# Optimization experiments

Measured on AMD Instinct MI355X. Metric: run time of the kernel, lower is better.

The kernel has to match this reference:

```python
import jax, jax.numpy as jnp
import numpy as np

C = 768
H = 12
T = 4096
B = 1
EPS = 1e-5


def setup_inputs() -> dict:
    key = jax.random.key(0)
    ks = jax.random.split(key, 16)
    s = 0.02
    return {
        "x": jax.random.normal(ks[0], (B, T, C), jnp.float32),
        "ln1_w": jnp.ones((C,), jnp.float32),
        "ln1_b": jnp.zeros((C,), jnp.float32),
        "W_attn": jax.random.normal(ks[1], (C, 3 * C), jnp.float32) * s,
        "b_attn": jnp.zeros((3 * C,), jnp.float32),
        "W_proj": jax.random.normal(ks[2], (C, C), jnp.float32) * s,
        "b_proj": jnp.zeros((C,), jnp.float32),
        "ln2_w": jnp.ones((C,), jnp.float32),
        "ln2_b": jnp.zeros((C,), jnp.float32),
        "W_fc": jax.random.normal(ks[3], (C, 4 * C), jnp.float32) * s,
        "b_fc": jnp.zeros((4 * C,), jnp.float32),
        "W_fc2": jax.random.normal(ks[4], (4 * C, C), jnp.float32) * s,
        "b_fc2": jnp.zeros((C,), jnp.float32),
    }


def _layernorm(x, w, b):
    mu = jnp.mean(x, axis=-1, keepdims=True)
    var = jnp.var(x, axis=-1, keepdims=True)
    return (x - mu) * jax.lax.rsqrt(var + EPS) * w + b


def _attn(x, W_attn, b_attn, W_proj, b_proj):
    Bb, Tt, Cc = x.shape
    hd = Cc // H
    qkv = x @ W_attn + b_attn                       # (B,T,3C)
    q, k, v = jnp.split(qkv, 3, axis=-1)
    q = q.reshape(Bb, Tt, H, hd).transpose(0, 2, 1, 3)  # (B,H,T,hd)
    k = k.reshape(Bb, Tt, H, hd).transpose(0, 2, 1, 3)
    v = v.reshape(Bb, Tt, H, hd).transpose(0, 2, 1, 3)
    att = jnp.einsum('bhqd,bhkd->bhqk', q, k) * (1.0 / np.sqrt(hd))
    causal = jnp.tril(jnp.ones((Tt, Tt), bool))
    att = jnp.where(causal, att, -jnp.inf)
    att = jax.nn.softmax(att, axis=-1)
    y = jnp.einsum('bhqk,bhkd->bhqd', att, v)       # (B,H,T,hd)
    y = y.transpose(0, 2, 1, 3).reshape(Bb, Tt, Cc)
    return y @ W_proj + b_proj


def _mlp(x, W_fc, b_fc, W_fc2, b_fc2):
    h = jax.nn.gelu(x @ W_fc + b_fc, approximate=False)
    return h @ W_fc2 + b_fc2


def reference(x, ln1_w, ln1_b, W_attn, b_attn, W_proj, b_proj,
              ln2_w, ln2_b, W_fc, b_fc, W_fc2, b_fc2):
    x = x + _attn(_layernorm(x, ln1_w, ln1_b), W_attn, b_attn, W_proj, b_proj)
    x = x + _mlp(_layernorm(x, ln2_w, ln2_b), W_fc, b_fc, W_fc2, b_fc2)
    return x
```

## Files before the change

### kernel.cpp

```cpp
#include <hip/hip_runtime.h>
#include <hip/hip_bf16.h>
#include <math.h>
#include <type_traits>

#define TSEQ 4096
#define CDIM 768
#define NH 12
#define HD 64

typedef float f32x4 __attribute__((ext_vector_type(4)));
typedef __bf16 bf16x8 __attribute__((ext_vector_type(8)));
typedef short s16x8 __attribute__((ext_vector_type(8)));
typedef uint u32x4 __attribute__((ext_vector_type(4)));

__device__ inline ushort f2bf(float f) {
  __hip_bfloat16 h = __float2bfloat16(f);
  return __builtin_bit_cast(ushort, h);
}

__device__ inline void async16(const void* g, void* l) {
  __builtin_amdgcn_global_load_lds(
      (__attribute__((address_space(1))) unsigned int*)(uintptr_t)g,
      (__attribute__((address_space(3))) unsigned int*)(uintptr_t)l, 16, 0, 0);
}

__device__ inline float exp2_fast(float x) {
  float r;
  asm volatile("v_exp_f32 %0, %1\n\ts_nop 0" : "=v"(r) : "v"(x));
  return r;
}

__device__ inline uint cvtpk(float a, float b) {
  uint r;
  asm volatile("v_cvt_pk_bf16_f32 %0, %1, %2" : "=v"(r) : "v"(a), "v"(b));
  return r;
}

__device__ inline bf16x8 frag_read(const ushort* base, int row, int kk, int lane) {
  const int byte = row * 128 + ((((kk * 4 + (lane >> 4)) ^ (row & 7))) << 4);
  return *(const bf16x8*)((const char*)base + byte);
}

__global__ __launch_bounds__(256) void wconv_t(
    const float* __restrict__ W, ushort* __restrict__ Wt, int K, int N)
{
  __shared__ float sm[32][33];
  const int n0 = blockIdx.x * 32, k0 = blockIdx.y * 32;
  const int c = threadIdx.x & 31, r0 = threadIdx.x >> 5;
#pragma unroll
  for (int i = 0; i < 4; ++i) {
    const int r = r0 + i * 8;
    sm[r][c] = W[(size_t)(k0 + r) * N + n0 + c];
  }
  __syncthreads();
#pragma unroll
  for (int i = 0; i < 4; ++i) {
    const int r = r0 + i * 8;
    Wt[(size_t)(n0 + r) * K + k0 + c] = f2bf(sm[c][r]);
  }
}

__global__ __launch_bounds__(256) void ln_kernel(
    const float* __restrict__ x, const float* __restrict__ w,
    const float* __restrict__ b, ushort* __restrict__ out)
{
  const int row = blockIdx.x;
  const int tid = threadIdx.x;
  const float* xr = x + (size_t)row * CDIM;
  float v[3];
  float s1 = 0.f, s2 = 0.f;
#pragma unroll
  for (int i = 0; i < 3; ++i) {
    v[i] = xr[tid + i * 256];
    s1 += v[i];
    s2 += v[i] * v[i];
  }
#pragma unroll
  for (int off = 32; off >= 1; off >>= 1) {
    s1 += __shfl_xor(s1, off, 64);
    s2 += __shfl_xor(s2, off, 64);
  }
  __shared__ float red1[4], red2[4];
  if ((tid & 63) == 0) { red1[tid >> 6] = s1; red2[tid >> 6] = s2; }
  __syncthreads();
  s1 = red1[0] + red1[1] + red1[2] + red1[3];
  s2 = red2[0] + red2[1] + red2[2] + red2[3];
  const float mu = s1 * (1.f / CDIM);
  const float var = s2 * (1.f / CDIM) - mu * mu;
  const float inv = rsqrtf(var + 1e-5f);
#pragma unroll
  for (int i = 0; i < 3; ++i) {
    const int c = tid + i * 256;
    out[(size_t)row * CDIM + c] = f2bf((v[i] - mu) * inv * w[c] + b[c]);
  }
}

template <int EPI, int BN>
__global__ __launch_bounds__(256) void gemm_bt(
    const ushort* __restrict__ A, const ushort* __restrict__ Bt,
    const float* __restrict__ bias, const float* __restrict__ res,
    ushort* __restrict__ outb, float* __restrict__ outf,
    int M, int N, int K, int gx)
{
  constexpr int NW = BN / 32;
  __shared__ __align__(16) ushort As[3][128 * 32];
  __shared__ __align__(16) ushort Bs[3][BN * 32];
  const int tid = threadIdx.x;
  const int lane = tid & 63;
  const int wv = tid >> 6;
  const int nwg = (int)gridDim.x;
  const int bid = (int)blockIdx.x;
  const int sw = (bid & 7) * (nwg >> 3) + (bid >> 3);
  const int rowBase = (sw / gx) * 128;
  const int colBase = (sw % gx) * BN;
  const int wr = (wv >> 1) * 64;
  const int wc = (wv & 1) * (BN / 2);

  f32x4 acc[4][NW] = {};

  const int e0 = tid * 8;
  const int r0 = e0 >> 5, c0 = e0 & 31;
  const int e1 = (tid + 256) * 8;
  const int r1 = e1 >> 5, c1 = e1 & 31;

  const ushort* Ag0 = A + (size_t)(rowBase + r0) * K + c0;
  const ushort* Ag1 = A + (size_t)(rowBase + r1) * K + c1;
  const ushort* Bg0 = Bt + (size_t)(colBase + r0) * K + c0;
  const ushort* Bg1 = Bt + (size_t)(colBase + r1) * K + c1;

  auto stage = [&](int buf, int k0) {
    async16(Ag0 + k0, &As[buf][e0]);
    async16(Ag1 + k0, &As[buf][e1]);
    async16(Bg0 + k0, &Bs[buf][e0]);
    if (BN == 128) async16(Bg1 + k0, &Bs[buf][e1]);
  };

  const int nt = K / 32;
  stage(0, 0);
  stage(1, 32);
  int b0 = 0, b1 = 1, b2 = 2;
  for (int t = 0; t < nt; ++t) {
    if (t < nt - 1) {
      if (BN == 128) asm volatile("s_waitcnt vmcnt(4)" ::: "memory");
      else           asm volatile("s_waitcnt vmcnt(3)" ::: "memory");
    } else {
      asm volatile("s_waitcnt vmcnt(0)" ::: "memory");
    }
    __builtin_amdgcn_sched_barrier(0);
    __builtin_amdgcn_s_barrier();
    __builtin_amdgcn_sched_barrier(0);
    if (t + 2 < nt) stage(b2, t * 32 + 64);

    bf16x8 af[4], bfr[NW];
#pragma unroll
    for (int m = 0; m < 4; ++m)
      af[m] = *(const bf16x8*)&As[b0][(wr + m * 16 + (lane & 15)) * 32 + (lane >> 4) * 8];
#pragma unroll
    for (int n = 0; n < NW; ++n)
      bfr[n] = *(const bf16x8*)&Bs[b0][(wc + n * 16 + (lane & 15)) * 32 + (lane >> 4) * 8];
    __builtin_amdgcn_s_setprio(1);
#pragma unroll
    for (int m = 0; m < 4; ++m)
#pragma unroll
      for (int n = 0; n < NW; ++n)
        acc[m][n] = __builtin_amdgcn_mfma_f32_16x16x32_bf16(af[m], bfr[n], acc[m][n], 0, 0, 0);
    __builtin_amdgcn_s_setprio(0);
    const int tmp = b0; b0 = b1; b1 = b2; b2 = tmp;
  }

#pragma unroll
  for (int n = 0; n < NW; ++n) {
    const int gc = colBase + wc + n * 16 + (lane & 15);
    const float bv = bias[gc];
#pragma unroll
    for (int m = 0; m < 4; ++m) {
#pragma unroll
      for (int j = 0; j < 4; ++j) {
        const int gr = rowBase + wr + m * 16 + (lane >> 4) * 4 + j;
        const float v = acc[m][n][j] + bv;
        if (EPI == 0) {
          outb[(size_t)gr * N + gc] = f2bf(v);
        } else if (EPI == 1) {
          outf[(size_t)gr * N + gc] = res[(size_t)gr * N + gc] + v;
        } else {
          const float g = 0.5f * v * (1.0f + erff(v * 0.70710678118654752f));
          outb[(size_t)gr * N + gc] = f2bf(g);
        }
      }
    }
  }
}

__global__ __launch_bounds__(256) void attn_kernel(
    const ushort* __restrict__ qkv, ushort* __restrict__ att)
{
  __shared__ __align__(16) ushort Ks[2][64 * 64];
  __shared__ __align__(16) ushort Vt[2][64 * 64];

  const int tid = threadIdx.x;
  const int lane = tid & 63;
  const int wv = tid >> 6;
  const int g = lane >> 4;
  const int ql = lane & 15;
  const int kh = wv & 1;
  const int qh = wv >> 1;
  const int p_ = blockIdx.x & 255, grp = blockIdx.x >> 8;
  const int item = (grp & 1) ? (grp * 256 + 255 - p_) : (grp * 256 + p_);
  const int qb = 63 - (item / 12);
  const int h = item % 12;
  const int t0 = qb * 64;
  const size_t rs = 3 * CDIM;
  const int qo = h * HD, ko = CDIM + h * HD, vo = 2 * CDIM + h * HD;

  const float cexp = 0.18033688f;
  const float cbias = -32.0f * 0.18033688f;

  const int L0 = tid * 16, L1 = (tid + 256) * 16;
  const int r_0 = L0 >> 7, c_0 = ((L0 >> 4) & 7) ^ (r_0 & 7);
  const int r_1 = L1 >> 7, c_1 = ((L1 >> 4) & 7) ^ (r_1 & 7);
  const ushort* kg0 = qkv + (size_t)r_0 * rs + ko + c_0 * 8;
  const ushort* kg1 = qkv + (size_t)r_1 * rs + ko + c_1 * 8;

  const int vt = (tid >> 3) * 2;
  const int vd = (tid & 7) * 8;
  const int s32 = vt & 31;
  const int col2 = (vt >> 5) * 64 + (8 * ((s32 >> 2) & 3) + 4 * (s32 >> 4) + (s32 & 3)) * 2;
  const ushort* vg = qkv + (size_t)vt * rs + vo + vd;

  bf16x8 qf[2][2];
#pragma unroll
  for (int qg = 0; qg < 2; ++qg) {
    const ushort* qrow = qkv + (size_t)(t0 + 32 * qh + 16 * qg + ql) * rs + qo + g * 8;
    qf[qg][0] = *(const bf16x8*)(qrow);
    qf[qg][1] = *(const bf16x8*)(qrow + 32);
  }

  s16x8 vA0 = *(const s16x8*)(vg);
  s16x8 vA1 = *(const s16x8*)(vg + rs);
  async16(kg0, (char*)Ks[0] + L0);
  async16(kg1, (char*)Ks[0] + L1);
#pragma unroll
  for (int jj = 0; jj < 8; ++jj) {
    const int d = vd + jj;
    const uint val = (uint)(ushort)vA0[jj] | ((uint)(ushort)vA1[jj] << 16);
    *(uint*)((char*)Vt[0] + d * 128 + (col2 ^ (((d >> 1) & 7) << 4))) = val;
  }

  f32x4 accO[2][4] = {};
  f32x4 accL[2] = {};
  const bf16x8 ones = __builtin_bit_cast(bf16x8,
      (u32x4){0x3F803F80u, 0x3F803F80u, 0x3F803F80u, 0x3F803F80u});
  const int swzv = (ql >> 1) & 7;

  int cur = 0;
  auto body = [&](int kb, int curb, auto diag_c) {
    constexpr bool DIAG = decltype(diag_c)::value;
    const size_t koff = (size_t)(kb + 1) * 64 * rs;

    if (!DIAG) {
      vA0 = *(const s16x8*)(vg + koff);
      vA1 = *(const s16x8*)(vg + koff + rs);
      asm volatile("s_waitcnt vmcnt(2) lgkmcnt(0)" ::: "memory");
    } else {
      asm volatile("s_waitcnt vmcnt(0) lgkmcnt(0)" ::: "memory");
    }
    __builtin_amdgcn_sched_barrier(0);
    __builtin_amdgcn_s_barrier();
    __builtin_amdgcn_sched_barrier(0);

    if (!DIAG) {
      async16(kg0 + koff, (char*)Ks[curb ^ 1] + L0);
      async16(kg1 + koff, (char*)Ks[curb ^ 1] + L1);
    }

    f32x4 accS[2][2] = {};
    __builtin_amdgcn_s_setprio(1);
#pragma unroll
    for (int kg = 0; kg < 2; ++kg)
#pragma unroll
      for (int kk = 0; kk < 2; ++kk) {
        const bf16x8 A = frag_read(Ks[curb], 32 * kh + 16 * kg + ql, kk, lane);
#pragma unroll
        for (int qg = 0; qg < 2; ++qg)
          accS[kg][qg] = __builtin_amdgcn_mfma_f32_16x16x32_bf16(
              A, qf[qg][kk], accS[kg][qg], 0, 0, 0);
      }
    __builtin_amdgcn_s_setprio(0);

    bf16x8 pa[2];
#pragma unroll
    for (int qg = 0; qg < 2; ++qg) {
      float e[2][4];
#pragma unroll
      for (int kg = 0; kg < 2; ++kg)
#pragma unroll
        for (int j = 0; j < 4; ++j) {
          float s = exp2_fast(fmaf(accS[kg][qg][j], cexp, cbias));
          if (DIAG && (32 * kh + 16 * kg + 4 * g + j) > (32 * qh + 16 * qg + ql)) s = 0.f;
          e[kg][j] = s;
        }
      const uint w0 = cvtpk(e[0][0], e[0][1]);
      const uint w1 = cvtpk(e[0][2], e[0][3]);
      const uint w2 = cvtpk(e[1][0], e[1][1]);
      const uint w3 = cvtpk(e[1][2], e[1][3]);
      pa[qg] = __builtin_bit_cast(bf16x8, (u32x4){w0, w1, w2, w3});
    }

    __builtin_amdgcn_s_setprio(1);
#pragma unroll
    for (int n = 0; n < 4; ++n) {
      const int byte = (16 * n + ql) * 128 + ((kh * 64 + 16 * g) ^ (swzv << 4));
      const bf16x8 bv = *(const bf16x8*)((const char*)Vt[curb] + byte);
#pragma unroll
      for (int qg = 0; qg < 2; ++qg)
        accO[qg][n] = __builtin_amdgcn_mfma_f32_16x16x32_bf16(pa[qg], bv, accO[qg][n], 0, 0, 0);
    }
#pragma unroll
    for (int qg = 0; qg < 2; ++qg)
      accL[qg] = __builtin_amdgcn_mfma_f32_16x16x32_bf16(pa[qg], ones, accL[qg], 0, 0, 0);
    __builtin_amdgcn_s_setprio(0);

    if (!DIAG) {
#pragma unroll
      for (int jj = 0; jj < 8; ++jj) {
        const int d = vd + jj;
        const uint val = (uint)(ushort)vA0[jj] | ((uint)(ushort)vA1[jj] << 16);
        *(uint*)((char*)Vt[curb ^ 1] + d * 128 + (col2 ^ (((d >> 1) & 7) << 4))) = val;
      }
    }
  };

  for (int kb = 0; kb < qb; ++kb) {
    body(kb, cur, std::false_type{});
    cur ^= 1;
  }
  body(qb, cur, std::true_type{});

  __syncthreads();
  float* mO = (float*)&Ks[0][0];
  float* mL = (float*)&Vt[0][0];
  if (kh == 1) {
#pragma unroll
    for (int qg = 0; qg < 2; ++qg) {
#pragma unroll
      for (int n = 0; n < 4; ++n)
        *(f32x4*)&mO[(((qh * 2 + qg) * 4 + n) * 64 + lane) * 4] = accO[qg][n];
      *(f32x4*)&mL[((qh * 2 + qg) * 64 + lane) * 4] = accL[qg];
    }
  }
  __syncthreads();
  if (kh == 0) {
#pragma unroll
    for (int qg = 0; qg < 2; ++qg) {
      const f32x4 ls = accL[qg] + *(const f32x4*)&mL[((qh * 2 + qg) * 64 + lane) * 4];
      f32x4 inv4;
#pragma unroll
      for (int jr = 0; jr < 4; ++jr) inv4[jr] = 1.0f / ls[jr];
#pragma unroll
      for (int n = 0; n < 4; ++n) {
        const f32x4 o = accO[qg][n] +
            *(const f32x4*)&mO[(((qh * 2 + qg) * 4 + n) * 64 + lane) * 4];
#pragma unroll
        for (int jr = 0; jr < 4; ++jr) {
          const int tq = t0 + 32 * qh + 16 * qg + 4 * g + jr;
          const int d = 16 * n + ql;
          att[(size_t)tq * CDIM + h * HD + d] = f2bf(o[jr] * inv4[jr]);
        }
      }
    }
  }
}

extern "C" void kernel_launch(void* const* d_in, const int* in_sizes, int n_in,
                              void* d_out, int out_size, void* d_ws, size_t ws_size,
                              hipStream_t stream)
{
  const float* x      = (const float*)d_in[0];
  const float* ln1_w  = (const float*)d_in[1];
  const float* ln1_b  = (const float*)d_in[2];
  const float* W_attn = (const float*)d_in[3];
  const float* b_attn = (const float*)d_in[4];
  const float* W_proj = (const float*)d_in[5];
  const float* b_proj = (const float*)d_in[6];
  const float* ln2_w  = (const float*)d_in[7];
  const float* ln2_b  = (const float*)d_in[8];
  const float* W_fc   = (const float*)d_in[9];
  const float* b_fc   = (const float*)d_in[10];
  const float* W_fc2  = (const float*)d_in[11];
  const float* b_fc2  = (const float*)d_in[12];
  float* out = (float*)d_out;

  char* base = (char*)d_ws;
  size_t off = 0;
  auto alloc = [&](size_t bytes) -> void* {
    void* q = base + off;
    off = (off + bytes + 255) & ~(size_t)255;
    return q;
  };
  ushort* Wt_attn = (ushort*)alloc(768ull * 2304 * 2);
  ushort* Wt_proj = (ushort*)alloc(768ull * 768 * 2);
  ushort* Wt_fc   = (ushort*)alloc(768ull * 3072 * 2);
  ushort* Wt_fc2  = (ushort*)alloc(3072ull * 768 * 2);
  ushort* t_ln    = (ushort*)alloc(4096ull * 768 * 2);
  ushort* t_att   = (ushort*)alloc(4096ull * 768 * 2);
  float*  t_x1    = (float*) alloc(4096ull * 768 * 4);
  ushort* t_big   = (ushort*)alloc(4096ull * 3072 * 2);
  ushort* t_qkv = t_big;
  ushort* t_h   = t_big;

  wconv_t<<<dim3(2304 / 32, 768 / 32), 256, 0, stream>>>(W_attn, Wt_attn, 768, 2304);
  wconv_t<<<dim3(768 / 32, 768 / 32), 256, 0, stream>>>(W_proj, Wt_proj, 768, 768);
  wconv_t<<<dim3(3072 / 32, 768 / 32), 256, 0, stream>>>(W_fc, Wt_fc, 768, 3072);
  wconv_t<<<dim3(768 / 32, 3072 / 32), 256, 0, stream>>>(W_fc2, Wt_fc2, 3072, 768);

  ln_kernel<<<4096, 256, 0, stream>>>(x, ln1_w, ln1_b, t_ln);
  gemm_bt<0, 128><<<18 * 32, 256, 0, stream>>>(
      t_ln, Wt_attn, b_attn, nullptr, t_qkv, nullptr, 4096, 2304, 768, 18);
  attn_kernel<<<dim3(768), 256, 0, stream>>>(t_qkv, t_att);
  gemm_bt<1, 64><<<12 * 32, 256, 0, stream>>>(
      t_att, Wt_proj, b_proj, x, nullptr, t_x1, 4096, 768, 768, 12);
  ln_kernel<<<4096, 256, 0, stream>>>(t_x1, ln2_w, ln2_b, t_ln);
  gemm_bt<2, 128><<<24 * 32, 256, 0, stream>>>(
      t_ln, Wt_fc, b_fc, nullptr, t_h, nullptr, 4096, 3072, 768, 24);
  gemm_bt<1, 64><<<12 * 32, 256, 0, stream>>>(
      t_h, Wt_fc2, b_fc2, t_x1, nullptr, out, 4096, 768, 3072, 12);
}
```

Before: 194.7 us.

## Write V transposed from QKV GEMM epilogue and read V fragments directly in attention

The QKV GEMM epilogue now writes the V columns in a transposed (head-dim-major) bf16 layout to a separate buffer. The attention kernel then loads V MFMA fragments straight from global memory instead of transposing V through LDS. The K tile gets a new swizzle and row mapping. The four weight-conversion kernels and the first layernorm are also merged into one prep launch to cut launch overhead. The cost is strided, uncoalesced 8-byte stores for V^T in the GEMM and global-latency V loads inside the attention loop, which now depend on manual vmcnt waits.

```diff
diff --git a/kernel.cpp b/kernel.cpp
--- a/kernel.cpp
+++ b/kernel.cpp
@@ -12,6 +12,7 @@
 typedef __bf16 bf16x8 __attribute__((ext_vector_type(8)));
 typedef short s16x8 __attribute__((ext_vector_type(8)));
 typedef uint u32x4 __attribute__((ext_vector_type(4)));
+typedef uint u32x2 __attribute__((ext_vector_type(2)));
 
 __device__ inline ushort f2bf(float f) {
   __hip_bfloat16 h = __float2bfloat16(f);
@@ -36,16 +37,28 @@
   return r;
 }
 
+__device__ inline u32x4 gload16(const void* p) {
+  u32x4 r;
+  asm volatile("global_load_dwordx4 %0, %1, off" : "=&v"(r) : "v"(p) : "memory");
+  return r;
+}
+
 __device__ inline bf16x8 frag_read(const ushort* base, int row, int kk, int lane) {
   const int byte = row * 128 + ((((kk * 4 + (lane >> 4)) ^ (row & 7))) << 4);
   return *(const bf16x8*)((const char*)base + byte);
 }
 
-__global__ __launch_bounds__(256) void wconv_t(
-    const float* __restrict__ W, ushort* __restrict__ Wt, int K, int N)
+__device__ inline bf16x8 frag_readK(const ushort* base, int row, int kk, int g) {
+  const int f = ((row & 3) << 1) | ((row >> 3) & 1);
+  const int byte = row * 128 + (((kk * 4 + g) ^ f) << 4);
+  return *(const bf16x8*)((const char*)base + byte);
+}
+
+__device__ void wconv_body(const float* __restrict__ W, ushort* __restrict__ Wt,
+                           int K, int N, int bx, int by)
 {
   __shared__ float sm[32][33];
-  const int n0 = blockIdx.x * 32, k0 = blockIdx.y * 32;
+  const int n0 = bx * 32, k0 = by * 32;
   const int c = threadIdx.x & 31, r0 = threadIdx.x >> 5;
 #pragma unroll
   for (int i = 0; i < 4; ++i) {
@@ -60,11 +73,9 @@
   }
 }
 
-__global__ __launch_bounds__(256) void ln_kernel(
-    const float* __restrict__ x, const float* __restrict__ w,
-    const float* __restrict__ b, ushort* __restrict__ out)
-{
-  const int row = blockIdx.x;
+__device__ void ln_body(const float* __restrict__ x, const float* __restrict__ w,
+                        const float* __restrict__ b, ushort* __restrict__ out, int row)
+{
   const int tid = threadIdx.x;
   const float* xr = x + (size_t)row * CDIM;
   float v[3];
@@ -90,9 +101,36 @@
   const float inv = rsqrtf(var + 1e-5f);
 #pragma unroll
   for (int i = 0; i < 3; ++i) {
-    const int c = tid + i * 256;
-    out[(size_t)row * CDIM + c] = f2bf((v[i] - mu) * inv * w[c] + b[c]);
-  }
+    const int c2 = tid + i * 256;
+    out[(size_t)row * CDIM + c2] = f2bf((v[i] - mu) * inv * w[c2] + b[c2]);
+  }
+}
+
+__global__ __launch_bounds__(256) void prep_kernel(
+    const float* __restrict__ W_attn, ushort* __restrict__ Wt_attn,
+    const float* __restrict__ W_proj, ushort* __restrict__ Wt_proj,
+    const float* __restrict__ W_fc,   ushort* __restrict__ Wt_fc,
+    const float* __restrict__ W_fc2,  ushort* __restrict__ Wt_fc2,
+    const float* __restrict__ x, const float* __restrict__ ln1w,
+    const float* __restrict__ ln1b, ushort* __restrict__ t_ln)
+{
+  int b = blockIdx.x;
+  if (b < 1728) { wconv_body(W_attn, Wt_attn, 768, 2304, b % 72, b / 72); return; }
+  b -= 1728;
+  if (b < 576)  { wconv_body(W_proj, Wt_proj, 768, 768, b % 24, b / 24); return; }
+  b -= 576;
+  if (b < 2304) { wconv_body(W_fc, Wt_fc, 768, 3072, b % 96, b / 96); return; }
+  b -= 2304;
+  if (b < 2304) { wconv_body(W_fc2, Wt_fc2, 3072, 768, b % 24, b / 24); return; }
+  b -= 2304;
+  ln_body(x, ln1w, ln1b, t_ln, b);
+}
+
+__global__ __launch_bounds__(256) void ln_kernel(
+    const float* __restrict__ x, const float* __restrict__ w,
+    const float* __restrict__ b, ushort* __restrict__ out)
+{
+  ln_body(x, w, b, out, blockIdx.x);
 }
 
 template <int EPI, int BN>
@@ -100,7 +138,7 @@
     const ushort* __restrict__ A, const ushort* __restrict__ Bt,
     const float* __restrict__ bias, const float* __restrict__ res,
     ushort* __restrict__ outb, float* __restrict__ outf,
-    int M, int N, int K, int gx)
+    int M, int N, int K, int gx, ushort* __restrict__ vTout)
 {
   constexpr int NW = BN / 32;
   __shared__ __align__(16) ushort As[3][128 * 32];
@@ -168,6 +206,24 @@
     const int tmp = b0; b0 = b1; b1 = b2; b2 = tmp;
   }
 
+  if (EPI == 0 && vTout != nullptr && colBase >= 1536) {
+#pragma unroll
+    for (int n = 0; n < NW; ++n) {
+      const int gc = colBase + wc + n * 16 + (lane & 15);
+      const float bv = bias[gc];
+      const size_t cp = (size_t)(gc - 1536) * 4096;
+#pragma unroll
+      for (int m = 0; m < 4; ++m) {
+        const int gr0 = rowBase + wr + m * 16 + (lane >> 4) * 4;
+        u32x2 pk;
+        pk.x = cvtpk(acc[m][n][0] + bv, acc[m][n][1] + bv);
+        pk.y = cvtpk(acc[m][n][2] + bv, acc[m][n][3] + bv);
+        *(u32x2*)&vTout[cp + gr0] = pk;
+      }
+    }
+    return;
+  }
+
 #pragma unroll
   for (int n = 0; n < NW; ++n) {
     const int gc = colBase + wc + n * 16 + (lane & 15);
@@ -192,10 +248,10 @@
 }
 
 __global__ __launch_bounds__(256) void attn_kernel(
-    const ushort* __restrict__ qkv, ushort* __restrict__ att)
-{
-  __shared__ __align__(16) ushort Ks[2][64 * 64];
-  __shared__ __align__(16) ushort Vt[2][64 * 64];
+    const ushort* __restrict__ qkv, const ushort* __restrict__ vT,
+    ushort* __restrict__ att)
+{
+  __shared__ __align__(16) char smem[20480];
 
   const int tid = threadIdx.x;
   const int lane = tid & 63;
@@ -210,22 +266,18 @@
   const int h = item % 12;
   const int t0 = qb * 64;
   const size_t rs = 3 * CDIM;
-  const int qo = h * HD, ko = CDIM + h * HD, vo = 2 * CDIM + h * HD;
+  const int qo = h * HD, ko = CDIM + h * HD;
 
   const float cexp = 0.18033688f;
   const float cbias = -32.0f * 0.18033688f;
 
   const int L0 = tid * 16, L1 = (tid + 256) * 16;
-  const int r_0 = L0 >> 7, c_0 = ((L0 >> 4) & 7) ^ (r_0 & 7);
-  const int r_1 = L1 >> 7, c_1 = ((L1 >> 4) & 7) ^ (r_1 & 7);
+  const int r_0 = L0 >> 7, c_0 = ((L0 >> 4) & 7) ^ (((r_0 & 3) << 1) | ((r_0 >> 3) & 1));
+  const int r_1 = L1 >> 7, c_1 = ((L1 >> 4) & 7) ^ (((r_1 & 3) << 1) | ((r_1 >> 3) & 1));
   const ushort* kg0 = qkv + (size_t)r_0 * rs + ko + c_0 * 8;
   const ushort* kg1 = qkv + (size_t)r_1 * rs + ko + c_1 * 8;
 
-  const int vt = (tid >> 3) * 2;
-  const int vd = (tid & 7) * 8;
-  const int s32 = vt & 31;
-  const int col2 = (vt >> 5) * 64 + (8 * ((s32 >> 2) & 3) + 4 * (s32 >> 4) + (s32 & 3)) * 2;
-  const ushort* vg = qkv + (size_t)vt * rs + vo + vd;
+  const ushort* vB = vT + (size_t)(h * 64 + ql) * 4096 + 32 * kh + 8 * g;
 
   bf16x8 qf[2][2];
 #pragma unroll
@@ -235,42 +287,34 @@
     qf[qg][1] = *(const bf16x8*)(qrow + 32);
   }
 
-  s16x8 vA0 = *(const s16x8*)(vg);
-  s16x8 vA1 = *(const s16x8*)(vg + rs);
-  async16(kg0, (char*)Ks[0] + L0);
-  async16(kg1, (char*)Ks[0] + L1);
-#pragma unroll
-  for (int jj = 0; jj < 8; ++jj) {
-    const int d = vd + jj;
-    const uint val = (uint)(ushort)vA0[jj] | ((uint)(ushort)vA1[jj] << 16);
-    *(uint*)((char*)Vt[0] + d * 128 + (col2 ^ (((d >> 1) & 7) << 4))) = val;
-  }
+  async16(kg0, smem + L0);
+  async16(kg1, smem + L1);
 
   f32x4 accO[2][4] = {};
   f32x4 accL[2] = {};
   const bf16x8 ones = __builtin_bit_cast(bf16x8,
       (u32x4){0x3F803F80u, 0x3F803F80u, 0x3F803F80u, 0x3F803F80u});
-  const int swzv = (ql >> 1) & 7;
-
-  int cur = 0;
-  auto body = [&](int kb, int curb, auto diag_c) {
+
+  auto body = [&](int kb, int curb, auto first_c, auto diag_c) {
+    constexpr bool FIRST = decltype(first_c)::value;
     constexpr bool DIAG = decltype(diag_c)::value;
-    const size_t koff = (size_t)(kb + 1) * 64 * rs;
-
-    if (!DIAG) {
-      vA0 = *(const s16x8*)(vg + koff);
-      vA1 = *(const s16x8*)(vg + koff + rs);
-      asm volatile("s_waitcnt vmcnt(2) lgkmcnt(0)" ::: "memory");
-    } else {
-      asm volatile("s_waitcnt vmcnt(0) lgkmcnt(0)" ::: "memory");
-    }
+    const ushort* Kt = (const ushort*)(smem + curb * 8192);
+
+    u32x4 vfr[4];
+#pragma unroll
+    for (int n = 0; n < 4; ++n)
+      vfr[n] = gload16(vB + (size_t)kb * 64 + (size_t)n * 16 * 4096);
+
+    if (FIRST) asm volatile("s_waitcnt vmcnt(0)" ::: "memory");
+    else       asm volatile("s_waitcnt vmcnt(4)" ::: "memory");
     __builtin_amdgcn_sched_barrier(0);
     __builtin_amdgcn_s_barrier();
     __builtin_amdgcn_sched_barrier(0);
 
     if (!DIAG) {
-      async16(kg0 + koff, (char*)Ks[curb ^ 1] + L0);
-      async16(kg1 + koff, (char*)Ks[curb ^ 1] + L1);
+      const size_t koff = (size_t)(kb + 1) * 64 * rs;
+      async16(kg0 + koff, smem + (curb ^ 1) * 8192 + L0);
+      async16(kg1 + koff, smem + (curb ^ 1) * 8192 + L1);
     }
 
     f32x4 accS[2][2] = {};
@@ -279,7 +323,7 @@
     for (int kg = 0; kg < 2; ++kg)
 #pragma unroll
       for (int kk = 0; kk < 2; ++kk) {
-        const bf16x8 A = frag_read(Ks[curb], 32 * kh + 16 * kg + ql, kk, lane);
+        const bf16x8 A = frag_readK(Kt, 32 * kh + 8 * (ql >> 2) + 4 * kg + (ql & 3), kk, g);
 #pragma unroll
         for (int qg = 0; qg < 2; ++qg)
           accS[kg][qg] = __builtin_amdgcn_mfma_f32_16x16x32_bf16(
@@ -296,7 +340,7 @@
 #pragma unroll
         for (int j = 0; j < 4; ++j) {
           float s = exp2_fast(fmaf(accS[kg][qg][j], cexp, cbias));
-          if (DIAG && (32 * kh + 16 * kg + 4 * g + j) > (32 * qh + 16 * qg + ql)) s = 0.f;
+          if (DIAG && (32 * kh + 8 * g + 4 * kg + j) > (32 * qh + 16 * qg + ql)) s = 0.f;
           e[kg][j] = s;
         }
       const uint w0 = cvtpk(e[0][0], e[0][1]);
@@ -306,11 +350,14 @@
       pa[qg] = __builtin_bit_cast(bf16x8, (u32x4){w0, w1, w2, w3});
     }
 
+    if (DIAG) asm volatile("s_waitcnt vmcnt(0)" ::: "memory");
+    else      asm volatile("s_waitcnt vmcnt(2)" ::: "memory");
+    __builtin_amdgcn_sched_barrier(0);
+
     __builtin_amdgcn_s_setprio(1);
 #pragma unroll
     for (int n = 0; n < 4; ++n) {
-      const int byte = (16 * n + ql) * 128 + ((kh * 64 + 16 * g) ^ (swzv << 4));
-      const bf16x8 bv = *(const bf16x8*)((const char*)Vt[curb] + byte);
+      const bf16x8 bv = __builtin_bit_cast(bf16x8, vfr[n]);
 #pragma unroll
       for (int qg = 0; qg < 2; ++qg)
         accO[qg][n] = __builtin_amdgcn_mfma_f32_16x16x32_bf16(pa[qg], bv, accO[qg][n], 0, 0, 0);
@@ -319,26 +366,23 @@
     for (int qg = 0; qg < 2; ++qg)
       accL[qg] = __builtin_amdgcn_mfma_f32_16x16x32_bf16(pa[qg], ones, accL[qg], 0, 0, 0);
     __builtin_amdgcn_s_setprio(0);
-
-    if (!DIAG) {
-#pragma unroll
-      for (int jj = 0; jj < 8; ++jj) {
-        const int d = vd + jj;
-        const uint val = (uint)(ushort)vA0[jj] | ((uint)(ushort)vA1[jj] << 16);
-        *(uint*)((char*)Vt[curb ^ 1] + d * 128 + (col2 ^ (((d >> 1) & 7) << 4))) = val;
-      }
-    }
   };
 
-  for (int kb = 0; kb < qb; ++kb) {
-    body(kb, cur, std::false_type{});
-    cur ^= 1;
-  }
-  body(qb, cur, std::true_type{});
+  if (qb == 0) {
+    body(0, 0, std::true_type{}, std::true_type{});
+  } else {
+    body(0, 0, std::true_type{}, std::false_type{});
+    int cur = 1;
+    for (int kb = 1; kb < qb; ++kb) {
+      body(kb, cur, std::false_type{}, std::false_type{});
+      cur ^= 1;
+    }
+    body(qb, cur, std::false_type{}, std::true_type{});
+  }
 
   __syncthreads();
-  float* mO = (float*)&Ks[0][0];
-  float* mL = (float*)&Vt[0][0];
+  float* mO = (float*)smem;
+  float* mL = (float*)(smem + 16384);
   if (kh == 1) {
 #pragma unroll
     for (int qg = 0; qg < 2; ++qg) {
@@ -406,22 +450,20 @@
   float*  t_x1    = (float*) alloc(4096ull * 768 * 4);
   ushort* t_big   = (ushort*)alloc(4096ull * 3072 * 2);
   ushort* t_qkv = t_big;
+  ushort* t_vT  = t_big + 4096ull * 2304;
   ushort* t_h   = t_big;
 
-  wconv_t<<<dim3(2304 / 32, 768 / 32), 256, 0, stream>>>(W_attn, Wt_attn, 768, 2304);
-  wconv_t<<<dim3(768 / 32, 768 / 32), 256, 0, stream>>>(W_proj, Wt_proj, 768, 768);
-  wconv_t<<<dim3(3072 / 32, 768 / 32), 256, 0, stream>>>(W_fc, Wt_fc, 768, 3072);
-  wconv_t<<<dim3(768 / 32, 3072 / 32), 256, 0, stream>>>(W_fc2, Wt_fc2, 3072, 768);
-
-  ln_kernel<<<4096, 256, 0, stream>>>(x, ln1_w, ln1_b, t_ln);
+  prep_kernel<<<11008, 256, 0, stream>>>(
+      W_attn, Wt_attn, W_proj, Wt_proj, W_fc, Wt_fc, W_fc2, Wt_fc2,
+      x, ln1_w, ln1_b, t_ln);
   gemm_bt<0, 128><<<18 * 32, 256, 0, stream>>>(
-      t_ln, Wt_attn, b_attn, nullptr, t_qkv, nullptr, 4096, 2304, 768, 18);
-  attn_kernel<<<dim3(768), 256, 0, stream>>>(t_qkv, t_att);
+      t_ln, Wt_attn, b_attn, nullptr, t_qkv, nullptr, 4096, 2304, 768, 18, t_vT);
+  attn_kernel<<<dim3(768), 256, 0, stream>>>(t_qkv, t_vT, t_att);
   gemm_bt<1, 64><<<12 * 32, 256, 0, stream>>>(
-      t_att, Wt_proj, b_proj, x, nullptr, t_x1, 4096, 768, 768, 12);
+      t_att, Wt_proj, b_proj, x, nullptr, t_x1, 4096, 768, 768, 12, nullptr);
   ln_kernel<<<4096, 256, 0, stream>>>(t_x1, ln2_w, ln2_b, t_ln);
   gemm_bt<2, 128><<<24 * 32, 256, 0, stream>>>(
-      t_ln, Wt_fc, b_fc, nullptr, t_h, nullptr, 4096, 3072, 768, 24);
+      t_ln, Wt_fc, b_fc, nullptr, t_h, nullptr, 4096, 3072, 768, 24, nullptr);
   gemm_bt<1, 64><<<12 * 32, 256, 0, stream>>>(
-      t_h, Wt_fc2, b_fc2, t_x1, nullptr, out, 4096, 768, 3072, 12);
-}
+      t_h, Wt_fc2, b_fc2, t_x1, nullptr, out, 4096, 768, 3072, 12, nullptr);
+}
```

Result: no change. 195.5 us (+0.4%).

## Merge weight conversions and first layernorm into one prep kernel; drop setprio

Applied to the files above, without the earlier changes.

Combines the four weight transpose/convert launches and the first layernorm into a single prep_kernel that dispatches on a flattened block index, removing four kernel launches and the idle gaps between them. It also removes s_setprio raising around the MFMA sections in the GEMM and attention kernels. The merged kernel mixes blocks with different shared-memory use and work sizes, and dropping the priority hints may change wave interleaving between the MFMA and memory phases.

```diff
diff --git a/kernel.cpp b/kernel.cpp
--- a/kernel.cpp
+++ b/kernel.cpp
@@ -41,11 +41,11 @@
   return *(const bf16x8*)((const char*)base + byte);
 }
 
-__global__ __launch_bounds__(256) void wconv_t(
-    const float* __restrict__ W, ushort* __restrict__ Wt, int K, int N)
+__device__ void wconv_body(const float* __restrict__ W, ushort* __restrict__ Wt,
+                           int K, int N, int bx, int by)
 {
   __shared__ float sm[32][33];
-  const int n0 = blockIdx.x * 32, k0 = blockIdx.y * 32;
+  const int n0 = bx * 32, k0 = by * 32;
   const int c = threadIdx.x & 31, r0 = threadIdx.x >> 5;
 #pragma unroll
   for (int i = 0; i < 4; ++i) {
@@ -60,11 +60,9 @@
   }
 }
 
-__global__ __launch_bounds__(256) void ln_kernel(
-    const float* __restrict__ x, const float* __restrict__ w,
-    const float* __restrict__ b, ushort* __restrict__ out)
-{
-  const int row = blockIdx.x;
+__device__ void ln_body(const float* __restrict__ x, const float* __restrict__ w,
+                        const float* __restrict__ b, ushort* __restrict__ out, int row)
+{
   const int tid = threadIdx.x;
   const float* xr = x + (size_t)row * CDIM;
   float v[3];
@@ -90,9 +88,36 @@
   const float inv = rsqrtf(var + 1e-5f);
 #pragma unroll
   for (int i = 0; i < 3; ++i) {
-    const int c = tid + i * 256;
-    out[(size_t)row * CDIM + c] = f2bf((v[i] - mu) * inv * w[c] + b[c]);
-  }
+    const int c2 = tid + i * 256;
+    out[(size_t)row * CDIM + c2] = f2bf((v[i] - mu) * inv * w[c2] + b[c2]);
+  }
+}
+
+__global__ __launch_bounds__(256) void prep_kernel(
+    const float* __restrict__ W_attn, ushort* __restrict__ Wt_attn,
+    const float* __restrict__ W_proj, ushort* __restrict__ Wt_proj,
+    const float* __restrict__ W_fc,   ushort* __restrict__ Wt_fc,
+    const float* __restrict__ W_fc2,  ushort* __restrict__ Wt_fc2,
+    const float* __restrict__ x, const float* __restrict__ ln1w,
+    const float* __restrict__ ln1b, ushort* __restrict__ t_ln)
+{
+  int b = blockIdx.x;
+  if (b < 1728) { wconv_body(W_attn, Wt_attn, 768, 2304, b % 72, b / 72); return; }
+  b -= 1728;
+  if (b < 576)  { wconv_body(W_proj, Wt_proj, 768, 768, b % 24, b / 24); return; }
+  b -= 576;
+  if (b < 2304) { wconv_body(W_fc, Wt_fc, 768, 3072, b % 96, b / 96); return; }
+  b -= 2304;
+  if (b < 2304) { wconv_body(W_fc2, Wt_fc2, 3072, 768, b % 24, b / 24); return; }
+  b -= 2304;
+  ln_body(x, ln1w, ln1b, t_ln, b);
+}
+
+__global__ __launch_bounds__(256) void ln_kernel(
+    const float* __restrict__ x, const float* __restrict__ w,
+    const float* __restrict__ b, ushort* __restrict__ out)
+{
+  ln_body(x, w, b, out, blockIdx.x);
 }
 
 template <int EPI, int BN>
@@ -158,13 +183,11 @@
 #pragma unroll
     for (int n = 0; n < NW; ++n)
       bfr[n] = *(const bf16x8*)&Bs[b0][(wc + n * 16 + (lane & 15)) * 32 + (lane >> 4) * 8];
-    __builtin_amdgcn_s_setprio(1);
 #pragma unroll
     for (int m = 0; m < 4; ++m)
 #pragma unroll
       for (int n = 0; n < NW; ++n)
         acc[m][n] = __builtin_amdgcn_mfma_f32_16x16x32_bf16(af[m], bfr[n], acc[m][n], 0, 0, 0);
-    __builtin_amdgcn_s_setprio(0);
     const int tmp = b0; b0 = b1; b1 = b2; b2 = tmp;
   }
 
@@ -274,7 +297,6 @@
     }
 
     f32x4 accS[2][2] = {};
-    __builtin_amdgcn_s_setprio(1);
 #pragma unroll
     for (int kg = 0; kg < 2; ++kg)
 #pragma unroll
@@ -285,7 +307,6 @@
           accS[kg][qg] = __builtin_amdgcn_mfma_f32_16x16x32_bf16(
               A, qf[qg][kk], accS[kg][qg], 0, 0, 0);
       }
-    __builtin_amdgcn_s_setprio(0);
 
     bf16x8 pa[2];
 #pragma unroll
@@ -306,7 +327,6 @@
       pa[qg] = __builtin_bit_cast(bf16x8, (u32x4){w0, w1, w2, w3});
     }
 
-    __builtin_amdgcn_s_setprio(1);
 #pragma unroll
     for (int n = 0; n < 4; ++n) {
       const int byte = (16 * n + ql) * 128 + ((kh * 64 + 16 * g) ^ (swzv << 4));
@@ -318,7 +338,6 @@
 #pragma unroll
     for (int qg = 0; qg < 2; ++qg)
       accL[qg] = __builtin_amdgcn_mfma_f32_16x16x32_bf16(pa[qg], ones, accL[qg], 0, 0, 0);
-    __builtin_amdgcn_s_setprio(0);
 
     if (!DIAG) {
 #pragma unroll
@@ -408,12 +427,9 @@
   ushort* t_qkv = t_big;
   ushort* t_h   = t_big;
 
-  wconv_t<<<dim3(2304 / 32, 768 / 32), 256, 0, stream>>>(W_attn, Wt_attn, 768, 2304);
-  wconv_t<<<dim3(768 / 32, 768 / 32), 256, 0, stream>>>(W_proj, Wt_proj, 768, 768);
-  wconv_t<<<dim3(3072 / 32, 768 / 32), 256, 0, stream>>>(W_fc, Wt_fc, 768, 3072);
-  wconv_t<<<dim3(768 / 32, 3072 / 32), 256, 0, stream>>>(W_fc2, Wt_fc2, 3072, 768);
-
-  ln_kernel<<<4096, 256, 0, stream>>>(x, ln1_w, ln1_b, t_ln);
+  prep_kernel<<<11008, 256, 0, stream>>>(
+      W_attn, Wt_attn, W_proj, Wt_proj, W_fc, Wt_fc, W_fc2, Wt_fc2,
+      x, ln1_w, ln1_b, t_ln);
   gemm_bt<0, 128><<<18 * 32, 256, 0, stream>>>(
       t_ln, Wt_attn, b_attn, nullptr, t_qkv, nullptr, 4096, 2304, 768, 18);
   attn_kernel<<<dim3(768), 256, 0, stream>>>(t_qkv, t_att);
```

Result: faster. 189.1 us (-2.9%).
